# Kernel optimization log

Measured on AMD Instinct MI355X. Metric: run time of the kernel, lower is better.

Reference implementation:

```python
import jax, jax.numpy as jnp
import numpy as np

ADDITIONAL_NOISE_STD = 0.1
RANDOM_MASK_FRACTION = 0.25
MASK_FILL_VALUE = 0.0


def setup_inputs() -> dict:
    key = jax.random.key(0)
    k1, k2, k3 = jax.random.split(key, 3)
    shape = (32, 1024, 2048)  # [batch, steps, obs_dim]
    data = jax.random.normal(k1, shape, dtype=jnp.float32)
    noise = jax.random.normal(k2, shape, dtype=jnp.float32)       # unit normal; scaled by std inside reference
    rand_vals = jax.random.uniform(k3, shape, dtype=jnp.float32)  # uniforms driving the topk mask
    return {"data": data, "noise": noise, "rand_vals": rand_vals}


def reference(data, noise, rand_vals):
    # apply_additional_noise: data + N(0, std)
    noisy = data + ADDITIONAL_NOISE_STD * noise

    # apply_random_mask along last dim:
    D = data.shape[-1]
    k = int(D * RANDOM_MASK_FRACTION)  # n_masked_per_step = 512
    _, idx = jax.lax.top_k(rand_vals, k)  # indices of k largest uniforms per row -> (B, S, k)

    # scatter True at topk indices (equivalent of torch scatter_ on a zero bool mask)
    B = data.shape[0] * data.shape[1]
    idx2 = idx.reshape(B, k)
    rows = jnp.arange(B)[:, None]
    mask = jnp.zeros((B, D), dtype=bool).at[rows, idx2].set(True).reshape(data.shape)

    masked = jnp.where(mask, jnp.asarray(MASK_FILL_VALUE, noisy.dtype), noisy)  # masked_fill
    mask_inverse = (~mask).astype(jnp.float32)  # logical_not(mask).float()
    return masked, mask_inverse
```

## Files before the change

### kernel.cpp

```cpp
#include <hip/hip_runtime.h>
#include <stdint.h>

#define D      2048
#define KSEL   512
#define CHUNKS 8

typedef float    f4 __attribute__((ext_vector_type(4)));
typedef unsigned u4 __attribute__((ext_vector_type(4)));

__device__ __forceinline__ int wave_sum_i(int v) {
    #pragma unroll
    for (int o = 32; o > 0; o >>= 1) v += __shfl_xor(v, o, 64);
    return v;
}
__device__ __forceinline__ unsigned wave_min_u(unsigned v) {
    #pragma unroll
    for (int o = 32; o > 0; o >>= 1) { unsigned t = __shfl_xor((int)v, o, 64); v = (t < v) ? t : v; }
    return v;
}
__device__ __forceinline__ unsigned wave_max_u(unsigned v) {
    #pragma unroll
    for (int o = 32; o > 0; o >>= 1) { unsigned t = __shfl_xor((int)v, o, 64); v = (t > v) ? t : v; }
    return v;
}

__device__ __forceinline__ int count_ge(const u4* r, unsigned p) {
    int c = 0;
    #pragma unroll
    for (int i = 0; i < CHUNKS; ++i) {
        c += (int)(r[i][0] >= p) + (int)(r[i][1] >= p) + (int)(r[i][2] >= p) + (int)(r[i][3] >= p);
    }
    return wave_sum_i(c);
}
__device__ __forceinline__ int count_eq(const u4* r, unsigned p) {
    int c = 0;
    #pragma unroll
    for (int i = 0; i < CHUNKS; ++i) {
        c += (int)(r[i][0] == p) + (int)(r[i][1] == p) + (int)(r[i][2] == p) + (int)(r[i][3] == p);
    }
    return wave_sum_i(c);
}
__device__ __forceinline__ unsigned min_ge(const u4* r, unsigned lo) {
    unsigned m = 0xFFFFFFFFu;
    #pragma unroll
    for (int i = 0; i < CHUNKS; ++i) {
        unsigned a;
        a = r[i][0]; if (a >= lo && a < m) m = a;
        a = r[i][1]; if (a >= lo && a < m) m = a;
        a = r[i][2]; if (a >= lo && a < m) m = a;
        a = r[i][3]; if (a >= lo && a < m) m = a;
    }
    return wave_min_u(m);
}
__device__ __forceinline__ unsigned max_in(const u4* r, unsigned lo, unsigned hi) {
    unsigned m = 0u;
    #pragma unroll
    for (int i = 0; i < CHUNKS; ++i) {
        unsigned a;
        a = r[i][0]; if (a >= lo && a <= hi && a > m) m = a;
        a = r[i][1]; if (a >= lo && a <= hi && a > m) m = a;
        a = r[i][2]; if (a >= lo && a <= hi && a > m) m = a;
        a = r[i][3]; if (a >= lo && a <= hi && a > m) m = a;
    }
    return wave_max_u(m);
}

__global__ __launch_bounds__(256, 6)
void BaseObservationModel_42923903156755_kernel(
    const float* __restrict__ data, const float* __restrict__ noise,
    const float* __restrict__ rand_vals, float* __restrict__ out,
    long long n_elems)
{
    const int lane = threadIdx.x & 63;
    const long long rows = n_elems / D;
    const long long row  = (long long)blockIdx.x * 4 + (threadIdx.x >> 6);
    if (row >= rows) return;
    const long long base = row * D;

    const u4* rp = (const u4*)(rand_vals + base);
    const f4* dp = (const f4*)(data + base);
    const f4* np = (const f4*)(noise + base);
    f4* op = (f4*)(out + base);
    f4* ip = (f4*)(out + n_elems + base);

    u4 rb[CHUNKS];
    #pragma unroll
    for (int i = 0; i < CHUNKS; ++i) rb[i] = __builtin_nontemporal_load(rp + i * 64 + lane);

    f4 d0 = __builtin_nontemporal_load(dp + 0 * 64 + lane);
    f4 n0 = __builtin_nontemporal_load(np + 0 * 64 + lane);
    f4 d1 = __builtin_nontemporal_load(dp + 1 * 64 + lane);
    f4 n1 = __builtin_nontemporal_load(np + 1 * 64 + lane);

    unsigned lo = 0u, hi = 0x3F7FFFFFu;
    int cnt_lo = D, cnt_hi1 = 0;
    unsigned T; int need2; int cnteq;
    int it = 0;
    for (;;) {
        if (cnt_lo == KSEL) {
            T = min_ge(rb, lo);
            cnteq = count_eq(rb, T);
            need2 = cnteq;
            break;
        }
        if (cnt_hi1 == KSEL - 1) {
            T = max_in(rb, lo, hi);
            cnteq = count_eq(rb, T);
            need2 = 1;
            break;
        }
        if (lo == hi) {
            T = lo;
            cnteq = cnt_lo - cnt_hi1;
            need2 = KSEL - cnt_hi1;
            break;
        }
        unsigned mid;
        if (it & 1) {
            mid = lo + ((hi - lo + 1) >> 1);
        } else {
            float lof = __uint_as_float(lo);
            float hif = __uint_as_float(hi + 1);
            float frac = (float)(cnt_lo - KSEL) / (float)(cnt_lo - cnt_hi1);
            float mf = lof + frac * (hif - lof);
            mid = __float_as_uint(mf);
            if (mid < lo + 1) mid = lo + 1;
            if (mid > hi)     mid = hi;
        }
        int c = count_ge(rb, mid);
        if (c >= KSEL) { lo = mid; cnt_lo = c; }
        else           { hi = mid - 1; cnt_hi1 = c; }
        ++it;
    }

    const bool fast = (need2 == cnteq);
    int rank_base = 0;

    #pragma unroll
    for (int i = 0; i < CHUNKS; ++i) {
        f4 dn, nn;
        if (i + 2 < CHUNKS) {
            dn = __builtin_nontemporal_load(dp + (i + 2) * 64 + lane);
            nn = __builtin_nontemporal_load(np + (i + 2) * 64 + lane);
        }

        const u4 rv = rb[i];
        bool m0, m1, m2, m3;
        if (fast) {
            m0 = rv[0] >= T; m1 = rv[1] >= T; m2 = rv[2] >= T; m3 = rv[3] >= T;
        } else {
            const bool e0 = (rv[0] == T), e1 = (rv[1] == T), e2 = (rv[2] == T), e3 = (rv[3] == T);
            int myc = (int)e0 + (int)e1 + (int)e2 + (int)e3;
            int inc = myc;
            #pragma unroll
            for (int o = 1; o < 64; o <<= 1) {
                int t = __shfl_up(inc, o, 64);
                if (lane >= o) inc += t;
            }
            int r = rank_base + inc - myc;
            m0 = (rv[0] > T) || (e0 && r < need2); r += (int)e0;
            m1 = (rv[1] > T) || (e1 && r < need2); r += (int)e1;
            m2 = (rv[2] > T) || (e2 && r < need2); r += (int)e2;
            m3 = (rv[3] > T) || (e3 && r < need2); r += (int)e3;
            rank_base += __shfl(inc, 63, 64);
        }

        const f4 d = d0, n = n0;
        f4 o4, i4;
        o4[0] = m0 ? 0.0f : fmaf(0.1f, n[0], d[0]);
        o4[1] = m1 ? 0.0f : fmaf(0.1f, n[1], d[1]);
        o4[2] = m2 ? 0.0f : fmaf(0.1f, n[2], d[2]);
        o4[3] = m3 ? 0.0f : fmaf(0.1f, n[3], d[3]);
        i4[0] = m0 ? 0.0f : 1.0f;
        i4[1] = m1 ? 0.0f : 1.0f;
        i4[2] = m2 ? 0.0f : 1.0f;
        i4[3] = m3 ? 0.0f : 1.0f;
        __builtin_nontemporal_store(o4, op + i * 64 + lane);
        __builtin_nontemporal_store(i4, ip + i * 64 + lane);

        d0 = d1; n0 = n1;
        if (i + 2 < CHUNKS) { d1 = dn; n1 = nn; }
    }
}

extern "C" void kernel_launch(void* const* d_in, const int* in_sizes, int n_in,
                              void* d_out, int out_size, void* d_ws, size_t ws_size,
                              hipStream_t stream) {
    const float* data      = (const float*)d_in[0];
    const float* noise     = (const float*)d_in[1];
    const float* rand_vals = (const float*)d_in[2];
    float* out = (float*)d_out;
    const long long n = (long long)in_sizes[0];
    const long long rows = n / D;
    const int blocks = (int)((rows + 3) / 4);
    BaseObservationModel_42923903156755_kernel<<<blocks, 256, 0, stream>>>(
        data, noise, rand_vals, out, n);
}
```

Measured before the change: 968.9 us.

## Split top-k selection and masked apply into two kernels via workspace bitmask

Splits the fused kernel into a selection kernel, which reads rand_vals, finds the threshold and writes a packed per-lane 32-bit mask word to workspace, and an apply kernel that streams data and noise and writes the outputs using that bitmask. Wave-wide counts now use ballot and popcount instead of shuffle reductions. The aim is to decouple the compute-heavy selection from the bandwidth-bound apply, so each kernel can run at higher occupancy. The cost is an extra launch and a small bitmask round trip, and the fused path is kept as a fallback when no workspace is available.

```diff
diff --git a/kernel.cpp b/kernel.cpp
--- a/kernel.cpp
+++ b/kernel.cpp
@@ -8,11 +8,6 @@
 typedef float    f4 __attribute__((ext_vector_type(4)));
 typedef unsigned u4 __attribute__((ext_vector_type(4)));
 
-__device__ __forceinline__ int wave_sum_i(int v) {
-    #pragma unroll
-    for (int o = 32; o > 0; o >>= 1) v += __shfl_xor(v, o, 64);
-    return v;
-}
 __device__ __forceinline__ unsigned wave_min_u(unsigned v) {
     #pragma unroll
     for (int o = 32; o > 0; o >>= 1) { unsigned t = __shfl_xor((int)v, o, 64); v = (t < v) ? t : v; }
@@ -28,17 +23,23 @@
     int c = 0;
     #pragma unroll
     for (int i = 0; i < CHUNKS; ++i) {
-        c += (int)(r[i][0] >= p) + (int)(r[i][1] >= p) + (int)(r[i][2] >= p) + (int)(r[i][3] >= p);
-    }
-    return wave_sum_i(c);
+        c += (int)__popcll(__ballot(r[i][0] >= p));
+        c += (int)__popcll(__ballot(r[i][1] >= p));
+        c += (int)__popcll(__ballot(r[i][2] >= p));
+        c += (int)__popcll(__ballot(r[i][3] >= p));
+    }
+    return c;
 }
 __device__ __forceinline__ int count_eq(const u4* r, unsigned p) {
     int c = 0;
     #pragma unroll
     for (int i = 0; i < CHUNKS; ++i) {
-        c += (int)(r[i][0] == p) + (int)(r[i][1] == p) + (int)(r[i][2] == p) + (int)(r[i][3] == p);
-    }
-    return wave_sum_i(c);
+        c += (int)__popcll(__ballot(r[i][0] == p));
+        c += (int)__popcll(__ballot(r[i][1] == p));
+        c += (int)__popcll(__ballot(r[i][2] == p));
+        c += (int)__popcll(__ballot(r[i][3] == p));
+    }
+    return c;
 }
 __device__ __forceinline__ unsigned min_ge(const u4* r, unsigned lo) {
     unsigned m = 0xFFFFFFFFu;
@@ -65,36 +66,9 @@
     return wave_max_u(m);
 }
 
-__global__ __launch_bounds__(256, 6)
-void BaseObservationModel_42923903156755_kernel(
-    const float* __restrict__ data, const float* __restrict__ noise,
-    const float* __restrict__ rand_vals, float* __restrict__ out,
-    long long n_elems)
-{
-    const int lane = threadIdx.x & 63;
-    const long long rows = n_elems / D;
-    const long long row  = (long long)blockIdx.x * 4 + (threadIdx.x >> 6);
-    if (row >= rows) return;
-    const long long base = row * D;
-
-    const u4* rp = (const u4*)(rand_vals + base);
-    const f4* dp = (const f4*)(data + base);
-    const f4* np = (const f4*)(noise + base);
-    f4* op = (f4*)(out + base);
-    f4* ip = (f4*)(out + n_elems + base);
-
-    u4 rb[CHUNKS];
-    #pragma unroll
-    for (int i = 0; i < CHUNKS; ++i) rb[i] = __builtin_nontemporal_load(rp + i * 64 + lane);
-
-    f4 d0 = __builtin_nontemporal_load(dp + 0 * 64 + lane);
-    f4 n0 = __builtin_nontemporal_load(np + 0 * 64 + lane);
-    f4 d1 = __builtin_nontemporal_load(dp + 1 * 64 + lane);
-    f4 n1 = __builtin_nontemporal_load(np + 1 * 64 + lane);
-
+__device__ __forceinline__ void select_topk(const u4* rb, unsigned& T, int& need2, int& cnteq) {
     unsigned lo = 0u, hi = 0x3F7FFFFFu;
     int cnt_lo = D, cnt_hi1 = 0;
-    unsigned T; int need2; int cnteq;
     int it = 0;
     for (;;) {
         if (cnt_lo == KSEL) {
@@ -132,18 +106,136 @@
         else           { hi = mid - 1; cnt_hi1 = c; }
         ++it;
     }
+}
+
+__global__ __launch_bounds__(256, 8)
+void BaseObservationModel_sel_kernel(
+    const float* __restrict__ rand_vals, unsigned* __restrict__ maskw,
+    long long n_elems)
+{
+    const int lane = threadIdx.x & 63;
+    const long long rows = n_elems / D;
+    const long long row  = (long long)blockIdx.x * 4 + (threadIdx.x >> 6);
+    if (row >= rows) return;
+
+    const u4* rp = (const u4*)(rand_vals + row * D);
+    u4 rb[CHUNKS];
+    #pragma unroll
+    for (int i = 0; i < CHUNKS; ++i) rb[i] = __builtin_nontemporal_load(rp + i * 64 + lane);
+
+    unsigned T; int need2, cnteq;
+    select_topk(rb, T, need2, cnteq);
+
+    const bool fast = (need2 == cnteq);
+    unsigned w = 0u;
+
+    if (fast) {
+        #pragma unroll
+        for (int i = 0; i < CHUNKS; ++i) {
+            const u4 rv = rb[i];
+            w |= (rv[0] >= T ? 1u : 0u) << (4 * i + 0);
+            w |= (rv[1] >= T ? 1u : 0u) << (4 * i + 1);
+            w |= (rv[2] >= T ? 1u : 0u) << (4 * i + 2);
+            w |= (rv[3] >= T ? 1u : 0u) << (4 * i + 3);
+        }
+    } else {
+        int rank_base = 0;
+        #pragma unroll
+        for (int i = 0; i < CHUNKS; ++i) {
+            const u4 rv = rb[i];
+            const bool e0 = (rv[0] == T), e1 = (rv[1] == T), e2 = (rv[2] == T), e3 = (rv[3] == T);
+            int myc = (int)e0 + (int)e1 + (int)e2 + (int)e3;
+            int inc = myc;
+            #pragma unroll
+            for (int o = 1; o < 64; o <<= 1) {
+                int t = __shfl_up(inc, o, 64);
+                if (lane >= o) inc += t;
+            }
+            int r = rank_base + inc - myc;
+            bool m0 = (rv[0] > T) || (e0 && r < need2); r += (int)e0;
+            bool m1 = (rv[1] > T) || (e1 && r < need2); r += (int)e1;
+            bool m2 = (rv[2] > T) || (e2 && r < need2); r += (int)e2;
+            bool m3 = (rv[3] > T) || (e3 && r < need2); r += (int)e3;
+            w |= (m0 ? 1u : 0u) << (4 * i + 0);
+            w |= (m1 ? 1u : 0u) << (4 * i + 1);
+            w |= (m2 ? 1u : 0u) << (4 * i + 2);
+            w |= (m3 ? 1u : 0u) << (4 * i + 3);
+            rank_base += __shfl(inc, 63, 64);
+        }
+    }
+    maskw[(row << 6) + lane] = w;
+}
+
+__global__ __launch_bounds__(256, 8)
+void BaseObservationModel_apply_kernel(
+    const float* __restrict__ data, const float* __restrict__ noise,
+    const unsigned* __restrict__ maskw, float* __restrict__ out,
+    long long n_elems)
+{
+    const int lane = threadIdx.x & 63;
+    const long long rows = n_elems / D;
+    const long long row  = (long long)blockIdx.x * 4 + (threadIdx.x >> 6);
+    if (row >= rows) return;
+    const long long base = row * D;
+
+    const f4* dp = (const f4*)(data + base);
+    const f4* np = (const f4*)(noise + base);
+    f4* op = (f4*)(out + base);
+    f4* ip = (f4*)(out + n_elems + base);
+
+    const unsigned w = maskw[(row << 6) + lane];
+
+    #pragma unroll
+    for (int i = 0; i < CHUNKS; ++i) {
+        const f4 d = __builtin_nontemporal_load(dp + i * 64 + lane);
+        const f4 n = __builtin_nontemporal_load(np + i * 64 + lane);
+        const unsigned b = (w >> (4 * i)) & 0xFu;
+        f4 o4, i4;
+        o4[0] = (b & 1u) ? 0.0f : fmaf(0.1f, n[0], d[0]);
+        o4[1] = (b & 2u) ? 0.0f : fmaf(0.1f, n[1], d[1]);
+        o4[2] = (b & 4u) ? 0.0f : fmaf(0.1f, n[2], d[2]);
+        o4[3] = (b & 8u) ? 0.0f : fmaf(0.1f, n[3], d[3]);
+        i4[0] = (b & 1u) ? 0.0f : 1.0f;
+        i4[1] = (b & 2u) ? 0.0f : 1.0f;
+        i4[2] = (b & 4u) ? 0.0f : 1.0f;
+        i4[3] = (b & 8u) ? 0.0f : 1.0f;
+        __builtin_nontemporal_store(o4, op + i * 64 + lane);
+        __builtin_nontemporal_store(i4, ip + i * 64 + lane);
+    }
+}
+
+__global__ __launch_bounds__(256, 6)
+void BaseObservationModel_fused_kernel(
+    const float* __restrict__ data, const float* __restrict__ noise,
+    const float* __restrict__ rand_vals, float* __restrict__ out,
+    long long n_elems)
+{
+    const int lane = threadIdx.x & 63;
+    const long long rows = n_elems / D;
+    const long long row  = (long long)blockIdx.x * 4 + (threadIdx.x >> 6);
+    if (row >= rows) return;
+    const long long base = row * D;
+
+    const u4* rp = (const u4*)(rand_vals + base);
+    const f4* dp = (const f4*)(data + base);
+    const f4* np = (const f4*)(noise + base);
+    f4* op = (f4*)(out + base);
+    f4* ip = (f4*)(out + n_elems + base);
+
+    u4 rb[CHUNKS];
+    #pragma unroll
+    for (int i = 0; i < CHUNKS; ++i) rb[i] = __builtin_nontemporal_load(rp + i * 64 + lane);
+
+    unsigned T; int need2, cnteq;
+    select_topk(rb, T, need2, cnteq);
 
     const bool fast = (need2 == cnteq);
     int rank_base = 0;
 
     #pragma unroll
     for (int i = 0; i < CHUNKS; ++i) {
-        f4 dn, nn;
-        if (i + 2 < CHUNKS) {
-            dn = __builtin_nontemporal_load(dp + (i + 2) * 64 + lane);
-            nn = __builtin_nontemporal_load(np + (i + 2) * 64 + lane);
-        }
-
+        const f4 d = __builtin_nontemporal_load(dp + i * 64 + lane);
+        const f4 n = __builtin_nontemporal_load(np + i * 64 + lane);
         const u4 rv = rb[i];
         bool m0, m1, m2, m3;
         if (fast) {
@@ -164,8 +256,6 @@
             m3 = (rv[3] > T) || (e3 && r < need2); r += (int)e3;
             rank_base += __shfl(inc, 63, 64);
         }
-
-        const f4 d = d0, n = n0;
         f4 o4, i4;
         o4[0] = m0 ? 0.0f : fmaf(0.1f, n[0], d[0]);
         o4[1] = m1 ? 0.0f : fmaf(0.1f, n[1], d[1]);
@@ -177,9 +267,6 @@
         i4[3] = m3 ? 0.0f : 1.0f;
         __builtin_nontemporal_store(o4, op + i * 64 + lane);
         __builtin_nontemporal_store(i4, ip + i * 64 + lane);
-
-        d0 = d1; n0 = n1;
-        if (i + 2 < CHUNKS) { d1 = dn; n1 = nn; }
     }
 }
 
@@ -193,6 +280,14 @@
     const long long n = (long long)in_sizes[0];
     const long long rows = n / D;
     const int blocks = (int)((rows + 3) / 4);
-    BaseObservationModel_42923903156755_kernel<<<blocks, 256, 0, stream>>>(
-        data, noise, rand_vals, out, n);
-}
+
+    const size_t mask_bytes = (size_t)rows * 64 * sizeof(unsigned);
+    if (d_ws != nullptr && ws_size >= mask_bytes) {
+        unsigned* maskw = (unsigned*)d_ws;
+        BaseObservationModel_sel_kernel<<<blocks, 256, 0, stream>>>(rand_vals, maskw, n);
+        BaseObservationModel_apply_kernel<<<blocks, 256, 0, stream>>>(data, noise, maskw, out, n);
+    } else {
+        BaseObservationModel_fused_kernel<<<blocks, 256, 0, stream>>>(
+            data, noise, rand_vals, out, n);
+    }
+}
```

Measured after the change: 975.9 us. About the same (+0.7%).
